# Kernel tuning notes

Hardware: AMD Instinct MI355X
Metric: run time of the kernel (lower is better)

The kernel has to match this reference:

```python
import jax, jax.numpy as jnp
import numpy as np
import math

HIDDEN = 1024
NUM_HEADS = 16
NUM_GROUPS = 16  # source einsum/rearrange only shape-checks when groups == heads
HEAD_DIM = HIDDEN // NUM_HEADS


def rope(x, base=10000.0):
    # x: [b, s, d]; applied to the FULL hidden vector before head split, as in source.
    # Source rope_fn has a reshape bug; this is the intended rotate-half RoPE with
    # half_d frequencies 1/base^(i/half_d) (== 1/base^(2i/d)).
    b, s, d = x.shape
    half = d // 2
    x1, x2 = x[..., :half], x[..., half:]
    pos = jnp.arange(s, dtype=x.dtype)[:, None]                          # [s,1]
    inv_freq = 1.0 / (base ** (jnp.arange(half, dtype=x.dtype) / half))  # [half]
    ang = pos * inv_freq[None, :]                                        # [s,half]
    sin = jnp.sin(ang)[None]                                             # [1,s,half]
    cos = jnp.cos(ang)[None]
    return jnp.concatenate([x1 * cos - x2 * sin, x2 * cos + x1 * sin], axis=-1)


def setup_inputs() -> dict:
    key = jax.random.key(0)
    ks = jax.random.split(key, 10)
    scale = 1.0 / math.sqrt(HIDDEN)
    inp = {
        "x": jax.random.normal(ks[0], (2, 2048, HIDDEN), dtype=jnp.float32),
        "attn_mask": jax.random.randint(ks[1], (2, 2048), 0, 2, dtype=jnp.int32),
        "Wq": jax.random.uniform(ks[2], (HIDDEN, HIDDEN), jnp.float32, -scale, scale),
        "bq": jax.random.uniform(ks[3], (HIDDEN,), jnp.float32, -scale, scale),
        "Wk": jax.random.uniform(ks[4], (HIDDEN, HIDDEN), jnp.float32, -scale, scale),
        "bk": jax.random.uniform(ks[5], (HIDDEN,), jnp.float32, -scale, scale),
        "Wv": jax.random.uniform(ks[6], (HIDDEN, HIDDEN), jnp.float32, -scale, scale),
        "bv": jax.random.uniform(ks[7], (HIDDEN,), jnp.float32, -scale, scale),
        "Wo": jax.random.uniform(ks[8], (HIDDEN, HIDDEN), jnp.float32, -scale, scale),
        "bo": jax.random.uniform(ks[9], (HIDDEN,), jnp.float32, -scale, scale),
    }
    return inp


def reference(x, attn_mask, Wq, bq, Wk, bk, Wv, bv, Wo, bo):
    b, s, _ = x.shape
    g = NUM_GROUPS
    subh = NUM_HEADS // g  # = 1 here
    d = HIDDEN // g        # per-group dim (== head dim when g == h)

    q = rope(x @ Wq.T + bq)
    k = rope(x @ Wk.T + bk)
    v = x @ Wv.T + bv

    # q: b s (g subh d) -> b g subh s d ; k,v: b s (g d) -> b g s d
    q = q.reshape(b, s, g, subh, d).transpose(0, 2, 3, 1, 4)
    k = k.reshape(b, s, g, d).transpose(0, 2, 1, 3)
    v = v.reshape(b, s, g, d).transpose(0, 2, 1, 3)

    e = jnp.einsum('bghqd,bgkd->bghqk', q, k) / math.sqrt(HEAD_DIM)  # [b,g,subh,s,s]
    mask5 = attn_mask[:, None, None, None, :]  # broadcast over g, subh, query
    e = jnp.where(mask5 == 0, -jnp.inf, e)
    attn = jax.nn.softmax(e, axis=-1)
    out = jnp.einsum('bghqk,bgkd->bghqd', attn, v)            # [b,g,subh,s,d]
    out = out.transpose(0, 3, 1, 2, 4).reshape(b, s, HIDDEN)  # b s (g subh d)
    return out @ Wo.T + bo
```

## Files before the change

### kernel.cpp

```cpp
#include <hip/hip_runtime.h>
#include <hip/hip_bf16.h>


constexpr int Bb  = 2;
constexpr int Ss  = 2048;
constexpr int Hh  = 1024;
constexpr int NHh = 16;
constexpr int Mm  = Bb * Ss;

typedef __attribute__((ext_vector_type(8))) unsigned short ushort8;
typedef __attribute__((ext_vector_type(4))) unsigned short ushort4_t;
typedef __attribute__((ext_vector_type(8))) short short8;
typedef __attribute__((ext_vector_type(4))) float f32x4;

__device__ __forceinline__ unsigned short f2bf(float f) {
    unsigned int u = __float_as_uint(f);
    u += 0x7fffu + ((u >> 16) & 1u);
    return (unsigned short)(u >> 16);
}
__device__ __forceinline__ float bf2f(unsigned short h) {
    return __uint_as_float(((unsigned int)h) << 16);
}
__device__ __forceinline__ void gload16(const void* g, void* l) {
    __builtin_amdgcn_global_load_lds(
        (const __attribute__((address_space(1))) unsigned int*)g,
        (__attribute__((address_space(3))) unsigned int*)l, 16, 0, 0);
}

__global__ __launch_bounds__(256) void convert_k(
    const float* __restrict__ x,
    const float* __restrict__ Wq, const float* __restrict__ Wk,
    const float* __restrict__ Wv, const float* __restrict__ Wo,
    unsigned short* __restrict__ xb, unsigned short* __restrict__ wall)
{
    size_t e = ((size_t)blockIdx.x * 256 + threadIdx.x) << 3;
    const float* s; unsigned short* d;
    if (e < (size_t)Mm * Hh) {
        s = x + e; d = xb + e;
    } else {
        size_t f = e - (size_t)Mm * Hh;
        int t = (int)(f >> 20);
        const float* w = (t == 0) ? Wq : (t == 1) ? Wk : (t == 2) ? Wv : Wo;
        s = w + (f & 1048575);
        d = wall + f;
    }
    float4 a = *(const float4*)s;
    float4 b = *(const float4*)(s + 4);
    ushort8 o;
    o[0] = f2bf(a.x); o[1] = f2bf(a.y); o[2] = f2bf(a.z); o[3] = f2bf(a.w);
    o[4] = f2bf(b.x); o[5] = f2bf(b.y); o[6] = f2bf(b.z); o[7] = f2bf(b.w);
    *(ushort8*)d = o;
}

#define GEMM_BODY(ATYPE_PTR, WPTR, K0MAX)                                          \
    __shared__ unsigned short As[128 * 64];                                        \
    __shared__ unsigned short Bs[128 * 64];                                        \
    const int tid  = threadIdx.x;                                                  \
    const int lane = tid & 63;                                                     \
    const int w    = tid >> 6;                                                     \
    const int wr   = w >> 1, wc = w & 1;                                           \
    const int l16  = lane & 15, g = lane >> 4;                                     \
    const int R0   = blockIdx.x * 128;                                             \
    char* asb = (char*)As; char* bsb = (char*)Bs;                                  \
    f32x4 acc[4][4] = {};                                                          \
    for (int k0 = 0; k0 < K0MAX; k0 += 64) {                                       \
        _Pragma("unroll")                                                          \
        for (int it = 0; it < 4; ++it) {                                           \
            int sbase = w * 4096 + it * 1024;                                      \
            int boff  = sbase + lane * 16;                                         \
            int r     = boff >> 7;                                                 \
            int c     = (boff >> 4) & 7;                                           \
            int col   = k0 + ((c ^ (r & 7)) << 3);                                 \
            gload16(&ATYPE_PTR[(size_t)(R0 + r) * 1024 + col], asb + sbase);       \
            gload16(&WPTR[(size_t)(gn + r) * 1024 + col], bsb + sbase);            \
        }                                                                          \
        __syncthreads();                                                           \
        short8 bfrag[4][2];                                                        \
        _Pragma("unroll")                                                          \
        for (int u = 0; u < 4; ++u) {                                              \
            int row = wc * 64 + u * 16 + l16;                                      \
            _Pragma("unroll")                                                      \
            for (int s = 0; s < 2; ++s)                                            \
                bfrag[u][s] = *(const short8*)(bsb + row * 128 +                   \
                               ((s * 64 + g * 16) ^ ((row & 7) << 4)));            \
        }                                                                          \
        _Pragma("unroll")                                                          \
        for (int t = 0; t < 4; ++t) {                                              \
            int row = wr * 64 + t * 16 + l16;                                      \
            short8 af[2];                                                          \
            _Pragma("unroll")                                                      \
            for (int s = 0; s < 2; ++s)                                            \
                af[s] = *(const short8*)(asb + row * 128 +                         \
                         ((s * 64 + g * 16) ^ ((row & 7) << 4)));                  \
            _Pragma("unroll")                                                      \
            for (int u = 0; u < 4; ++u) {                                          \
                acc[t][u] = __builtin_amdgcn_mfma_f32_16x16x32_bf16(af[0], bfrag[u][0], acc[t][u], 0, 0, 0); \
                acc[t][u] = __builtin_amdgcn_mfma_f32_16x16x32_bf16(af[1], bfrag[u][1], acc[t][u], 0, 0, 0); \
            }                                                                      \
        }                                                                          \
        __syncthreads();                                                           \
    }

__global__ __launch_bounds__(256) void gemm_qkv_k(
    const unsigned short* __restrict__ xb, const unsigned short* __restrict__ wall,
    const float* __restrict__ bq, const float* __restrict__ bk, const float* __restrict__ bv,
    unsigned short* __restrict__ q, unsigned short* __restrict__ k2,
    unsigned short* __restrict__ v)
{
    const int gn = blockIdx.y * 128;
    GEMM_BODY(xb, wall, 1024)

    const int sel = gn >> 10;
    const int n0  = gn & 1023;
    const float* bias = (sel == 0) ? bq : (sel == 1) ? bk : bv;
    unsigned short* outp = (sel == 0) ? q : (sel == 1) ? k2 : v;
    const float qs = (sel == 0) ? 0.18033688011112042f : 1.0f;
    #pragma unroll
    for (int u = 0; u < 4; ++u) {
        int coll = wc * 64 + u * 16 + l16;
        float bb = bias[n0 + coll];
        #pragma unroll
        for (int t = 0; t < 4; ++t)
            #pragma unroll
            for (int rr = 0; rr < 4; ++rr) {
                int row = R0 + wr * 64 + t * 16 + g * 4 + rr;
                outp[(size_t)row * 1024 + n0 + coll] = f2bf((acc[t][u][rr] + bb) * qs);
            }
    }
}

__global__ __launch_bounds__(256) void gemm_out_k(
    const unsigned short* __restrict__ ao, const unsigned short* __restrict__ wo,
    const float* __restrict__ bo, float* __restrict__ out)
{
    const int gn = blockIdx.y * 128;
    GEMM_BODY(ao, wo, 1024)

    #pragma unroll
    for (int u = 0; u < 4; ++u) {
        int coll = wc * 64 + u * 16 + l16;
        float bb = bo[gn + coll];
        #pragma unroll
        for (int t = 0; t < 4; ++t)
            #pragma unroll
            for (int rr = 0; rr < 4; ++rr) {
                int row = R0 + wr * 64 + t * 16 + g * 4 + rr;
                out[(size_t)row * 1024 + gn + coll] = acc[t][u][rr] + bb;
            }
    }
}

__global__ __launch_bounds__(256) void rope_k(
    unsigned short* __restrict__ q, unsigned short* __restrict__ kk)
{
    int idx = blockIdx.x * 256 + threadIdx.x;
    int row = idx >> 7;
    int j4  = (idx & 127) << 2;
    int pos = row & (Ss - 1);
    size_t base = (size_t)row * 1024;

    ushort4_t qa = *(ushort4_t*)&q[base + j4];
    ushort4_t qb = *(ushort4_t*)&q[base + 512 + j4];
    ushort4_t ka = *(ushort4_t*)&kk[base + j4];
    ushort4_t kb = *(ushort4_t*)&kk[base + 512 + j4];

    #pragma unroll
    for (int t = 0; t < 4; ++t) {
        float jj = (float)(j4 + t);
        float inv = exp2f(jj * -0.0259525632621414f);
        float ang = (float)pos * inv;
        float sn, cs;
        __sincosf(ang, &sn, &cs);
        float a = bf2f(qa[t]), b = bf2f(qb[t]);
        qa[t] = f2bf(a * cs - b * sn);
        qb[t] = f2bf(b * cs + a * sn);
        float c = bf2f(ka[t]), d = bf2f(kb[t]);
        ka[t] = f2bf(c * cs - d * sn);
        kb[t] = f2bf(d * cs + c * sn);
    }
    *(ushort4_t*)&q[base + j4]        = qa;
    *(ushort4_t*)&q[base + 512 + j4]  = qb;
    *(ushort4_t*)&kk[base + j4]       = ka;
    *(ushort4_t*)&kk[base + 512 + j4] = kb;
}

__global__ __launch_bounds__(256, 4) void flash_k(
    const unsigned short* __restrict__ q, const unsigned short* __restrict__ k,
    const unsigned short* __restrict__ v, const int* __restrict__ mask,
    unsigned short* __restrict__ ao)
{
    __shared__ unsigned short Ks[64 * 64];
    __shared__ unsigned short Vt[64 * 64];
    __shared__ unsigned short Pb[4][16 * 64];

    const int F   = blockIdx.x;
    const int xcd = F & 7, j = F >> 3;
    const int grp = xcd * 4 + (j >> 5);
    const int qb  = j & 31;
    const int h   = grp & 15;
    const int bz  = grp >> 4;

    const int tid  = threadIdx.x;
    const int lane = tid & 63;
    const int w    = tid >> 6;
    const int l16  = lane & 15;
    const int g    = lane >> 4;
    const int sw   = (lane & 7) << 4;

    char* ksb = (char*)&Ks[0];
    char* vtb = (char*)&Vt[0];
    char* pbb = (char*)&Pb[w][0];

    const int qrowbase = bz * Ss + qb * 64 + w * 16;

    short8 qf[2];
    #pragma unroll
    for (int s = 0; s < 2; ++s)
        qf[s] = *(const short8*)&q[(size_t)(qrowbase + l16) * 1024
                                   + h * 64 + s * 32 + g * 8];

    f32x4 O[4];
    #pragma unroll
    for (int d = 0; d < 4; ++d) O[d] = (f32x4)0.f;
    f32x4 Osum = (f32x4)0.f;
    float mrow = -1.0e4f;

    const float THR = 10.0f;

    short8 ones;
    #pragma unroll
    for (int e = 0; e < 8; ++e) ones[e] = (short)0x3F80;

    for (int kt = 0; kt < Ss / 64; ++kt) {
        #pragma unroll
        for (int it = 0; it < 2; ++it) {
            int cid = w * 128 + it * 64 + lane;
            int row = cid >> 3;
            int sub = cid & 7;
            gload16(&k[(size_t)(bz * Ss + kt * 64 + row) * 1024 + h * 64
                       + ((sub ^ (row & 7)) << 3)],
                    ksb + w * 2048 + it * 1024);
        }
        {
            int kv    = tid & 63;
            int dbase = (tid >> 6) << 4;
            #pragma unroll
            for (int half = 0; half < 2; ++half) {
                int d0 = dbase + half * 8;
                ushort8 t8 = *(const ushort8*)&v[(size_t)(bz * Ss + kt * 64 + kv) * 1024
                                                 + h * 64 + d0];
                #pragma unroll
                for (int jj = 0; jj < 8; ++jj) {
                    int d = d0 + jj;
                    *(unsigned short*)(vtb + d * 128 + ((kv * 2) ^ ((d & 7) << 4))) = t8[jj];
                }
            }
        }
        __syncthreads();

        f32x4 S[4];
        #pragma unroll
        for (int kt4 = 0; kt4 < 4; ++kt4) S[kt4] = (f32x4)0.f;
        #pragma unroll
        for (int kt4 = 0; kt4 < 4; ++kt4) {
            int key = kt4 * 16 + l16;
            short8 kf0 = *(const short8*)(ksb + key * 128 + ((g * 16) ^ sw));
            short8 kf1 = *(const short8*)(ksb + key * 128 + ((64 + g * 16) ^ sw));
            S[kt4] = __builtin_amdgcn_mfma_f32_16x16x32_bf16(kf0, qf[0], S[kt4], 0, 0, 0);
            S[kt4] = __builtin_amdgcn_mfma_f32_16x16x32_bf16(kf1, qf[1], S[kt4], 0, 0, 0);
        }

        int mk[4][4];
        #pragma unroll
        for (int kt4 = 0; kt4 < 4; ++kt4)
            *(int4*)&mk[kt4][0] = *(const int4*)&mask[bz * Ss + kt * 64 + kt4 * 16 + g * 4];
        #pragma unroll
        for (int kt4 = 0; kt4 < 4; ++kt4)
            #pragma unroll
            for (int r = 0; r < 4; ++r)
                S[kt4][r] = mk[kt4][r] ? S[kt4][r] : -1e30f;

        float m0 = fmaxf(fmaxf(S[0][0], S[0][1]), fmaxf(S[0][2], S[0][3]));
        float m1 = fmaxf(fmaxf(S[1][0], S[1][1]), fmaxf(S[1][2], S[1][3]));
        float m2 = fmaxf(fmaxf(S[2][0], S[2][1]), fmaxf(S[2][2], S[2][3]));
        float m3 = fmaxf(fmaxf(S[3][0], S[3][1]), fmaxf(S[3][2], S[3][3]));
        float m  = fmaxf(fmaxf(m0, m1), fmaxf(m2, m3));
        m = fmaxf(m, __shfl_xor(m, 16));
        m = fmaxf(m, __shfl_xor(m, 32));

        if (__any((int)(m > mrow + THR))) {
            float mn = fmaxf(mrow, m);
            float rs = exp2f(mrow - mn);
            mrow = mn;
            #pragma unroll
            for (int r = 0; r < 4; ++r) {
                float f0 = __shfl(rs, g * 4 + r);
                #pragma unroll
                for (int dt = 0; dt < 4; ++dt) O[dt][r] *= f0;
                Osum[r] *= f0;
            }
        }

        #pragma unroll
        for (int kt4 = 0; kt4 < 4; ++kt4) {
            float p0 = exp2f(S[kt4][0] - mrow);
            float p1 = exp2f(S[kt4][1] - mrow);
            float p2 = exp2f(S[kt4][2] - mrow);
            float p3 = exp2f(S[kt4][3] - mrow);
            unsigned int u01, u23;
            asm("v_cvt_pk_bf16_f32 %0, %1, %2" : "=v"(u01) : "v"(p0), "v"(p1));
            asm("v_cvt_pk_bf16_f32 %0, %1, %2" : "=v"(u23) : "v"(p2), "v"(p3));
            int pbyte = (kt4 * 32 + g * 8) ^ ((l16 & 7) << 4);
            *(uint2*)(pbb + l16 * 128 + pbyte) = make_uint2(u01, u23);
        }

        #pragma unroll
        for (int ks = 0; ks < 2; ++ks) {
            short8 pf = *(const short8*)(pbb + l16 * 128 + ((ks * 64 + g * 16) ^ sw));
            Osum = __builtin_amdgcn_mfma_f32_16x16x32_bf16(pf, ones, Osum, 0, 0, 0);
            #pragma unroll
            for (int dt = 0; dt < 4; ++dt) {
                short8 vf = *(const short8*)(vtb + (dt * 16 + l16) * 128 + ((ks * 64 + g * 16) ^ sw));
                O[dt] = __builtin_amdgcn_mfma_f32_16x16x32_bf16(pf, vf, O[dt], 0, 0, 0);
            }
        }
        __syncthreads();
    }

    #pragma unroll
    for (int r = 0; r < 4; ++r) {
        float inv = 1.0f / Osum[r];
        int row = qrowbase + g * 4 + r;
        #pragma unroll
        for (int dt = 0; dt < 4; ++dt)
            ao[(size_t)row * 1024 + h * 64 + dt * 16 + l16] = f2bf(O[dt][r] * inv);
    }
}

extern "C" void kernel_launch(void* const* d_in, const int* in_sizes, int n_in,
                              void* d_out, int out_size, void* d_ws, size_t ws_size,
                              hipStream_t stream)
{
    const float* x  = (const float*)d_in[0];
    const int*   am = (const int*)d_in[1];
    const float* Wq = (const float*)d_in[2];
    const float* bq = (const float*)d_in[3];
    const float* Wk = (const float*)d_in[4];
    const float* bk = (const float*)d_in[5];
    const float* Wv = (const float*)d_in[6];
    const float* bv = (const float*)d_in[7];
    const float* Wo = (const float*)d_in[8];
    const float* bo = (const float*)d_in[9];
    float* out = (float*)d_out;

    const size_t NE = (size_t)Mm * Hh;
    unsigned short* q    = (unsigned short*)d_ws;
    unsigned short* k    = q + NE;
    unsigned short* v    = k + NE;
    unsigned short* ao   = v + NE;
    unsigned short* xb   = ao + NE;
    unsigned short* wall = xb + NE;
    unsigned short* wo   = wall + 3u * 1048576u;

    convert_k<<<(2 * NE) / (256 * 8), 256, 0, stream>>>(x, Wq, Wk, Wv, Wo, xb, wall);
    gemm_qkv_k<<<dim3(Mm / 128, 3072 / 128), 256, 0, stream>>>(
        xb, wall, bq, bk, bv, q, k, v);
    rope_k<<<(Mm * 128) / 256, 256, 0, stream>>>(q, k);
    flash_k<<<dim3(Ss / 64 * NHh * Bb), 256, 0, stream>>>(q, k, v, am, ao);
    gemm_out_k<<<dim3(Mm / 128, Hh / 128), 256, 0, stream>>>(ao, wo, bo, out);
}
```

Measured before the change: 168.2 us.

## Pre-swizzle Q/K/V into MFMA fragment layout and register-pipeline flash attention

RoPE now also writes Q and K into an MFMA-fragment-ordered buffer, and a new kernel reorders V into transposed fragment order. This lets flash attention load K/V fragments straight from global memory into registers, double-buffering K across iterations, with no LDS and no barriers. Each warp now handles two 16-row query tiles (128 rows per block). P is repacked in registers with permlane swaps instead of an LDS round trip. The costs are an extra V pass, more workspace aliasing, higher register pressure (launch bounds min blocks lowered to 2), and half as many flash blocks.

Result: no change. 166.5 us (-1.0%).

```diff
diff --git a/kernel.cpp b/kernel.cpp
--- a/kernel.cpp
+++ b/kernel.cpp
@@ -9,9 +9,9 @@
 constexpr int Mm  = Bb * Ss;
 
 typedef __attribute__((ext_vector_type(8))) unsigned short ushort8;
-typedef __attribute__((ext_vector_type(4))) unsigned short ushort4_t;
 typedef __attribute__((ext_vector_type(8))) short short8;
 typedef __attribute__((ext_vector_type(4))) float f32x4;
+typedef __attribute__((ext_vector_type(4))) unsigned int u32x4;
 
 __device__ __forceinline__ unsigned short f2bf(float f) {
     unsigned int u = __float_as_uint(f);
@@ -150,53 +150,192 @@
     }
 }
 
-__global__ __launch_bounds__(256) void rope_k(
-    unsigned short* __restrict__ q, unsigned short* __restrict__ kk)
-{
-    int idx = blockIdx.x * 256 + threadIdx.x;
-    int row = idx >> 7;
-    int j4  = (idx & 127) << 2;
-    int pos = row & (Ss - 1);
-    size_t base = (size_t)row * 1024;
-
-    ushort4_t qa = *(ushort4_t*)&q[base + j4];
-    ushort4_t qb = *(ushort4_t*)&q[base + 512 + j4];
-    ushort4_t ka = *(ushort4_t*)&kk[base + j4];
-    ushort4_t kb = *(ushort4_t*)&kk[base + 512 + j4];
-
-    #pragma unroll
-    for (int t = 0; t < 4; ++t) {
-        float jj = (float)(j4 + t);
+__global__ __launch_bounds__(256) void rope_frag_k(
+    const unsigned short* __restrict__ qin, const unsigned short* __restrict__ kin,
+    unsigned short* __restrict__ qfrag, unsigned short* __restrict__ kfrag)
+{
+    __shared__ unsigned short Ld[2][64][72];
+    const int kt = blockIdx.x;
+    const int hp = blockIdx.y;
+    const int zz = blockIdx.z;
+    const int bz = zz & 1, sel = zz >> 1;
+    const unsigned short* src = sel ? kin : qin;
+    unsigned short* dstf = sel ? kfrag : qfrag;
+
+    const int t   = threadIdx.x;
+    const int r   = t & 63;
+    const int c16 = (t >> 6) << 4;
+    const int pos = kt * 64 + r;
+    const size_t rowb = (size_t)(bz * Ss + pos) * 1024;
+
+    ushort8 A0 = *(const ushort8*)&src[rowb + hp * 64 + c16];
+    ushort8 A1 = *(const ushort8*)&src[rowb + hp * 64 + c16 + 8];
+    ushort8 B0 = *(const ushort8*)&src[rowb + (hp + 8) * 64 + c16];
+    ushort8 B1 = *(const ushort8*)&src[rowb + (hp + 8) * 64 + c16 + 8];
+
+    #pragma unroll
+    for (int i = 0; i < 16; ++i) {
+        int d = c16 + i;
+        float jj  = (float)(hp * 64 + d);
         float inv = exp2f(jj * -0.0259525632621414f);
         float ang = (float)pos * inv;
         float sn, cs;
         __sincosf(ang, &sn, &cs);
-        float a = bf2f(qa[t]), b = bf2f(qb[t]);
-        qa[t] = f2bf(a * cs - b * sn);
-        qb[t] = f2bf(b * cs + a * sn);
-        float c = bf2f(ka[t]), d = bf2f(kb[t]);
-        ka[t] = f2bf(c * cs - d * sn);
-        kb[t] = f2bf(d * cs + c * sn);
-    }
-    *(ushort4_t*)&q[base + j4]        = qa;
-    *(ushort4_t*)&q[base + 512 + j4]  = qb;
-    *(ushort4_t*)&kk[base + j4]       = ka;
-    *(ushort4_t*)&kk[base + 512 + j4] = kb;
-}
-
-__global__ __launch_bounds__(256, 4) void flash_k(
-    const unsigned short* __restrict__ q, const unsigned short* __restrict__ k,
-    const unsigned short* __restrict__ v, const int* __restrict__ mask,
+        unsigned short ua = (i < 8) ? A0[i] : A1[i - 8];
+        unsigned short ub = (i < 8) ? B0[i] : B1[i - 8];
+        float a = bf2f(ua), b = bf2f(ub);
+        Ld[0][r][d] = f2bf(a * cs - b * sn);
+        Ld[1][r][d] = f2bf(b * cs + a * sn);
+    }
+    __syncthreads();
+
+    #pragma unroll
+    for (int cc = 0; cc < 4; ++cc) {
+        int c    = t * 4 + cc;
+        int hh   = c >> 9;
+        int ci   = c & 511;
+        int blk  = ci >> 7, s2 = (ci >> 6) & 1, lane2 = ci & 63;
+        int gg = lane2 >> 4, ll = lane2 & 15;
+        ushort8 o = *(const ushort8*)&Ld[hh][blk * 16 + ll][s2 * 32 + gg * 8];
+        size_t base = (size_t)(bz * 16 + hp + hh * 8) * 131072 + (size_t)kt * 4096;
+        *(ushort8*)&dstf[base + (size_t)ci * 8] = o;
+    }
+}
+
+__global__ __launch_bounds__(256) void fragify_v_k(
+    const unsigned short* __restrict__ v, unsigned short* __restrict__ vfrag)
+{
+    __shared__ unsigned short Ld[64][72];
+    const int kt = blockIdx.x, bh = blockIdx.y;
+    const int bz = bh >> 4, h = bh & 15;
+    const int t = threadIdx.x;
+    const int r = t & 63, c0 = (t >> 6) << 4;
+    const unsigned short* srcp = &v[(size_t)(bz * Ss + kt * 64 + r) * 1024 + h * 64 + c0];
+    *(ushort8*)&Ld[r][c0]     = *(const ushort8*)srcp;
+    *(ushort8*)&Ld[r][c0 + 8] = *(const ushort8*)(srcp + 8);
+    __syncthreads();
+
+    #pragma unroll
+    for (int cc = 0; cc < 2; ++cc) {
+        int c = t * 2 + cc;
+        int dt4 = c >> 7, ks = (c >> 6) & 1, lane2 = c & 63;
+        int gg = lane2 >> 4, ll = lane2 & 15;
+        ushort8 o;
+        #pragma unroll
+        for (int e = 0; e < 8; ++e)
+            o[e] = Ld[ks * 32 + gg * 8 + e][dt4 * 16 + ll];
+        *(ushort8*)&vfrag[(size_t)bh * 131072 + (size_t)kt * 4096 + (size_t)c * 8] = o;
+    }
+}
+
+#define FLASH_ITER(KC, KN, KT)                                                     \
+    {                                                                              \
+        const int ktn = ((KT) + 1) & 31;                                           \
+        _Pragma("unroll")                                                          \
+        for (int i = 0; i < 8; ++i)                                                \
+            KN[i] = *(const short8*)&kfb[(size_t)ktn * 4096 + i * 512 + lane * 8]; \
+        _Pragma("unroll")                                                          \
+        for (int i = 0; i < 8; ++i)                                                \
+            VV[i] = *(const short8*)&vfb[(size_t)(KT) * 4096 + i * 512 + lane * 8];\
+        int mk[4][4];                                                              \
+        _Pragma("unroll")                                                          \
+        for (int k4 = 0; k4 < 4; ++k4)                                             \
+            *(int4*)&mk[k4][0] =                                                   \
+                *(const int4*)&mask[bz * Ss + (KT) * 64 + k4 * 16 + g * 4];        \
+        f32x4 S[2][4];                                                             \
+        _Pragma("unroll")                                                          \
+        for (int t = 0; t < 2; ++t)                                                \
+            _Pragma("unroll")                                                      \
+            for (int k4 = 0; k4 < 4; ++k4) S[t][k4] = (f32x4)0.f;                  \
+        _Pragma("unroll")                                                          \
+        for (int k4 = 0; k4 < 4; ++k4)                                             \
+            _Pragma("unroll")                                                      \
+            for (int t = 0; t < 2; ++t) {                                          \
+                S[t][k4] = __builtin_amdgcn_mfma_f32_16x16x32_bf16(                \
+                    KC[k4 * 2 + 0], qf[t][0], S[t][k4], 0, 0, 0);                  \
+                S[t][k4] = __builtin_amdgcn_mfma_f32_16x16x32_bf16(                \
+                    KC[k4 * 2 + 1], qf[t][1], S[t][k4], 0, 0, 0);                  \
+            }                                                                      \
+        _Pragma("unroll")                                                          \
+        for (int t = 0; t < 2; ++t)                                                \
+            _Pragma("unroll")                                                      \
+            for (int k4 = 0; k4 < 4; ++k4)                                         \
+                _Pragma("unroll")                                                  \
+                for (int r = 0; r < 4; ++r)                                        \
+                    S[t][k4][r] = mk[k4][r] ? S[t][k4][r] : -1e30f;                \
+        float rm[2];                                                               \
+        _Pragma("unroll")                                                          \
+        for (int t = 0; t < 2; ++t) {                                              \
+            float m0 = fmaxf(fmaxf(S[t][0][0], S[t][0][1]), fmaxf(S[t][0][2], S[t][0][3])); \
+            float m1 = fmaxf(fmaxf(S[t][1][0], S[t][1][1]), fmaxf(S[t][1][2], S[t][1][3])); \
+            float m2 = fmaxf(fmaxf(S[t][2][0], S[t][2][1]), fmaxf(S[t][2][2], S[t][2][3])); \
+            float m3 = fmaxf(fmaxf(S[t][3][0], S[t][3][1]), fmaxf(S[t][3][2], S[t][3][3])); \
+            float m  = fmaxf(fmaxf(m0, m1), fmaxf(m2, m3));                        \
+            m = fmaxf(m, __shfl_xor(m, 16));                                       \
+            m = fmaxf(m, __shfl_xor(m, 32));                                       \
+            rm[t] = m;                                                             \
+        }                                                                          \
+        bool grow = (rm[0] > mrow[0] + 10.0f) || (rm[1] > mrow[1] + 10.0f);        \
+        if (__any((int)grow)) {                                                    \
+            float mn0 = fmaxf(mrow[0], rm[0]);                                     \
+            float mn1 = fmaxf(mrow[1], rm[1]);                                     \
+            float rs0 = exp2f(mrow[0] - mn0);                                      \
+            float rs1 = exp2f(mrow[1] - mn1);                                      \
+            mrow[0] = mn0; mrow[1] = mn1;                                          \
+            _Pragma("unroll")                                                      \
+            for (int r = 0; r < 4; ++r) {                                          \
+                float f0 = __shfl(rs0, g * 4 + r);                                 \
+                float f1 = __shfl(rs1, g * 4 + r);                                 \
+                _Pragma("unroll")                                                  \
+                for (int dt = 0; dt < 4; ++dt) { O[0][dt][r] *= f0; O[1][dt][r] *= f1; } \
+                Osum[0][r] *= f0; Osum[1][r] *= f1;                                \
+            }                                                                      \
+        }                                                                          \
+        _Pragma("unroll")                                                          \
+        for (int t = 0; t < 2; ++t) {                                              \
+            unsigned int U[4][2];                                                  \
+            _Pragma("unroll")                                                      \
+            for (int k4 = 0; k4 < 4; ++k4) {                                       \
+                float p0 = exp2f(S[t][k4][0] - mrow[t]);                           \
+                float p1 = exp2f(S[t][k4][1] - mrow[t]);                           \
+                float p2 = exp2f(S[t][k4][2] - mrow[t]);                           \
+                float p3 = exp2f(S[t][k4][3] - mrow[t]);                           \
+                asm("v_cvt_pk_bf16_f32 %0, %1, %2" : "=v"(U[k4][0]) : "v"(p0), "v"(p1)); \
+                asm("v_cvt_pk_bf16_f32 %0, %1, %2" : "=v"(U[k4][1]) : "v"(p2), "v"(p3)); \
+            }                                                                      \
+                \
+            asm("v_permlane32_swap_b32 %0, %1" : "+v"(U[0][0]), "+v"(U[1][0]));    \
+            asm("v_permlane32_swap_b32 %0, %1" : "+v"(U[0][1]), "+v"(U[1][1]));    \
+            asm("v_permlane32_swap_b32 %0, %1" : "+v"(U[2][0]), "+v"(U[3][0]));    \
+            asm("v_permlane32_swap_b32 %0, %1" : "+v"(U[2][1]), "+v"(U[3][1]));    \
+            asm("v_permlane16_swap_b32 %0, %1" : "+v"(U[0][0]), "+v"(U[1][0]));    \
+            asm("v_permlane16_swap_b32 %0, %1" : "+v"(U[0][1]), "+v"(U[1][1]));    \
+            asm("v_permlane16_swap_b32 %0, %1" : "+v"(U[2][0]), "+v"(U[3][0]));    \
+            asm("v_permlane16_swap_b32 %0, %1" : "+v"(U[2][1]), "+v"(U[3][1]));    \
+            _Pragma("unroll")                                                      \
+            for (int ks = 0; ks < 2; ++ks) {                                       \
+                u32x4 gp;                                                          \
+                gp[0] = U[2 * ks][0]; gp[1] = U[2 * ks][1];                        \
+                gp[2] = U[2 * ks + 1][0]; gp[3] = U[2 * ks + 1][1];                \
+                short8 pf = __builtin_bit_cast(short8, gp);                        \
+                Osum[t] = __builtin_amdgcn_mfma_f32_16x16x32_bf16(pf, ones, Osum[t], 0, 0, 0); \
+                _Pragma("unroll")                                                  \
+                for (int dt = 0; dt < 4; ++dt)                                     \
+                    O[t][dt] = __builtin_amdgcn_mfma_f32_16x16x32_bf16(            \
+                        pf, VV[dt * 2 + ks], O[t][dt], 0, 0, 0);                   \
+            }                                                                      \
+        }                                                                          \
+    }
+
+__global__ __launch_bounds__(256, 2) void flash_k(
+    const unsigned short* __restrict__ qfrag, const unsigned short* __restrict__ kfrag,
+    const unsigned short* __restrict__ vfrag, const int* __restrict__ mask,
     unsigned short* __restrict__ ao)
 {
-    __shared__ unsigned short Ks[64 * 64];
-    __shared__ unsigned short Vt[64 * 64];
-    __shared__ unsigned short Pb[4][16 * 64];
-
     const int F   = blockIdx.x;
     const int xcd = F & 7, j = F >> 3;
-    const int grp = xcd * 4 + (j >> 5);
-    const int qb  = j & 31;
+    const int grp = xcd * 4 + (j >> 4);
+    const int qb  = j & 15;
     const int h   = grp & 15;
     const int bz  = grp >> 4;
 
@@ -205,136 +344,55 @@
     const int w    = tid >> 6;
     const int l16  = lane & 15;
     const int g    = lane >> 4;
-    const int sw   = (lane & 7) << 4;
-
-    char* ksb = (char*)&Ks[0];
-    char* vtb = (char*)&Vt[0];
-    char* pbb = (char*)&Pb[w][0];
-
-    const int qrowbase = bz * Ss + qb * 64 + w * 16;
-
-    short8 qf[2];
-    #pragma unroll
-    for (int s = 0; s < 2; ++s)
-        qf[s] = *(const short8*)&q[(size_t)(qrowbase + l16) * 1024
-                                   + h * 64 + s * 32 + g * 8];
-
-    f32x4 O[4];
-    #pragma unroll
-    for (int d = 0; d < 4; ++d) O[d] = (f32x4)0.f;
-    f32x4 Osum = (f32x4)0.f;
-    float mrow = -1.0e4f;
-
-    const float THR = 10.0f;
+
+    const size_t fb = (size_t)(bz * 16 + h) * 131072;
+    const unsigned short* kfb = kfrag + fb;
+    const unsigned short* vfb = vfrag + fb;
+    const unsigned short* qfb = qfrag + fb;
+
+    const int qrowbase = bz * Ss + qb * 128 + w * 32;
+
+    short8 qf[2][2];
+    #pragma unroll
+    for (int t = 0; t < 2; ++t)
+        #pragma unroll
+        for (int s = 0; s < 2; ++s)
+            qf[t][s] = *(const short8*)&qfb[(size_t)(qb * 8 + w * 2 + t) * 1024
+                                            + s * 512 + lane * 8];
+
+    f32x4 O[2][4];
+    #pragma unroll
+    for (int t = 0; t < 2; ++t)
+        #pragma unroll
+        for (int d = 0; d < 4; ++d) O[t][d] = (f32x4)0.f;
+    f32x4 Osum[2];
+    Osum[0] = (f32x4)0.f; Osum[1] = (f32x4)0.f;
+    float mrow[2] = {-1.0e4f, -1.0e4f};
 
     short8 ones;
     #pragma unroll
     for (int e = 0; e < 8; ++e) ones[e] = (short)0x3F80;
 
-    for (int kt = 0; kt < Ss / 64; ++kt) {
-        #pragma unroll
-        for (int it = 0; it < 2; ++it) {
-            int cid = w * 128 + it * 64 + lane;
-            int row = cid >> 3;
-            int sub = cid & 7;
-            gload16(&k[(size_t)(bz * Ss + kt * 64 + row) * 1024 + h * 64
-                       + ((sub ^ (row & 7)) << 3)],
-                    ksb + w * 2048 + it * 1024);
+    short8 KA[8], KB[8], VV[8];
+    #pragma unroll
+    for (int i = 0; i < 8; ++i)
+        KA[i] = *(const short8*)&kfb[(size_t)i * 512 + lane * 8];
+
+    for (int kt = 0; kt < 32; kt += 2) {
+        FLASH_ITER(KA, KB, kt)
+        FLASH_ITER(KB, KA, kt + 1)
+    }
+
+    #pragma unroll
+    for (int t = 0; t < 2; ++t)
+        #pragma unroll
+        for (int r = 0; r < 4; ++r) {
+            float inv = 1.0f / Osum[t][r];
+            int row = qrowbase + t * 16 + g * 4 + r;
+            #pragma unroll
+            for (int dt = 0; dt < 4; ++dt)
+                ao[(size_t)row * 1024 + h * 64 + dt * 16 + l16] = f2bf(O[t][dt][r] * inv);
         }
-        {
-            int kv    = tid & 63;
-            int dbase = (tid >> 6) << 4;
-            #pragma unroll
-            for (int half = 0; half < 2; ++half) {
-                int d0 = dbase + half * 8;
-                ushort8 t8 = *(const ushort8*)&v[(size_t)(bz * Ss + kt * 64 + kv) * 1024
-                                                 + h * 64 + d0];
-                #pragma unroll
-                for (int jj = 0; jj < 8; ++jj) {
-                    int d = d0 + jj;
-                    *(unsigned short*)(vtb + d * 128 + ((kv * 2) ^ ((d & 7) << 4))) = t8[jj];
-                }
-            }
-        }
-        __syncthreads();
-
-        f32x4 S[4];
-        #pragma unroll
-        for (int kt4 = 0; kt4 < 4; ++kt4) S[kt4] = (f32x4)0.f;
-        #pragma unroll
-        for (int kt4 = 0; kt4 < 4; ++kt4) {
-            int key = kt4 * 16 + l16;
-            short8 kf0 = *(const short8*)(ksb + key * 128 + ((g * 16) ^ sw));
-            short8 kf1 = *(const short8*)(ksb + key * 128 + ((64 + g * 16) ^ sw));
-            S[kt4] = __builtin_amdgcn_mfma_f32_16x16x32_bf16(kf0, qf[0], S[kt4], 0, 0, 0);
-            S[kt4] = __builtin_amdgcn_mfma_f32_16x16x32_bf16(kf1, qf[1], S[kt4], 0, 0, 0);
-        }
-
-        int mk[4][4];
-        #pragma unroll
-        for (int kt4 = 0; kt4 < 4; ++kt4)
-            *(int4*)&mk[kt4][0] = *(const int4*)&mask[bz * Ss + kt * 64 + kt4 * 16 + g * 4];
-        #pragma unroll
-        for (int kt4 = 0; kt4 < 4; ++kt4)
-            #pragma unroll
-            for (int r = 0; r < 4; ++r)
-                S[kt4][r] = mk[kt4][r] ? S[kt4][r] : -1e30f;
-
-        float m0 = fmaxf(fmaxf(S[0][0], S[0][1]), fmaxf(S[0][2], S[0][3]));
-        float m1 = fmaxf(fmaxf(S[1][0], S[1][1]), fmaxf(S[1][2], S[1][3]));
-        float m2 = fmaxf(fmaxf(S[2][0], S[2][1]), fmaxf(S[2][2], S[2][3]));
-        float m3 = fmaxf(fmaxf(S[3][0], S[3][1]), fmaxf(S[3][2], S[3][3]));
-        float m  = fmaxf(fmaxf(m0, m1), fmaxf(m2, m3));
-        m = fmaxf(m, __shfl_xor(m, 16));
-        m = fmaxf(m, __shfl_xor(m, 32));
-
-        if (__any((int)(m > mrow + THR))) {
-            float mn = fmaxf(mrow, m);
-            float rs = exp2f(mrow - mn);
-            mrow = mn;
-            #pragma unroll
-            for (int r = 0; r < 4; ++r) {
-                float f0 = __shfl(rs, g * 4 + r);
-                #pragma unroll
-                for (int dt = 0; dt < 4; ++dt) O[dt][r] *= f0;
-                Osum[r] *= f0;
-            }
-        }
-
-        #pragma unroll
-        for (int kt4 = 0; kt4 < 4; ++kt4) {
-            float p0 = exp2f(S[kt4][0] - mrow);
-            float p1 = exp2f(S[kt4][1] - mrow);
-            float p2 = exp2f(S[kt4][2] - mrow);
-            float p3 = exp2f(S[kt4][3] - mrow);
-            unsigned int u01, u23;
-            asm("v_cvt_pk_bf16_f32 %0, %1, %2" : "=v"(u01) : "v"(p0), "v"(p1));
-            asm("v_cvt_pk_bf16_f32 %0, %1, %2" : "=v"(u23) : "v"(p2), "v"(p3));
-            int pbyte = (kt4 * 32 + g * 8) ^ ((l16 & 7) << 4);
-            *(uint2*)(pbb + l16 * 128 + pbyte) = make_uint2(u01, u23);
-        }
-
-        #pragma unroll
-        for (int ks = 0; ks < 2; ++ks) {
-            short8 pf = *(const short8*)(pbb + l16 * 128 + ((ks * 64 + g * 16) ^ sw));
-            Osum = __builtin_amdgcn_mfma_f32_16x16x32_bf16(pf, ones, Osum, 0, 0, 0);
-            #pragma unroll
-            for (int dt = 0; dt < 4; ++dt) {
-                short8 vf = *(const short8*)(vtb + (dt * 16 + l16) * 128 + ((ks * 64 + g * 16) ^ sw));
-                O[dt] = __builtin_amdgcn_mfma_f32_16x16x32_bf16(pf, vf, O[dt], 0, 0, 0);
-            }
-        }
-        __syncthreads();
-    }
-
-    #pragma unroll
-    for (int r = 0; r < 4; ++r) {
-        float inv = 1.0f / Osum[r];
-        int row = qrowbase + g * 4 + r;
-        #pragma unroll
-        for (int dt = 0; dt < 4; ++dt)
-            ao[(size_t)row * 1024 + h * 64 + dt * 16 + l16] = f2bf(O[dt][r] * inv);
-    }
 }
 
 extern "C" void kernel_launch(void* const* d_in, const int* in_sizes, int n_in,
@@ -354,18 +412,22 @@
     float* out = (float*)d_out;
 
     const size_t NE = (size_t)Mm * Hh;
-    unsigned short* q    = (unsigned short*)d_ws;
-    unsigned short* k    = q + NE;
-    unsigned short* v    = k + NE;
-    unsigned short* ao   = v + NE;
-    unsigned short* xb   = ao + NE;
-    unsigned short* wall = xb + NE;
-    unsigned short* wo   = wall + 3u * 1048576u;
+    unsigned short* q     = (unsigned short*)d_ws;
+    unsigned short* k     = q + NE;
+    unsigned short* v     = k + NE;
+    unsigned short* ao    = v + NE;
+    unsigned short* xb    = ao + NE;
+    unsigned short* wall  = xb + NE;
+    unsigned short* wo    = wall + 3u * 1048576u;
+    unsigned short* kfrag = wall + 4u * 1048576u;
+    unsigned short* qfrag = xb;
+    unsigned short* vfrag = q;
 
     convert_k<<<(2 * NE) / (256 * 8), 256, 0, stream>>>(x, Wq, Wk, Wv, Wo, xb, wall);
     gemm_qkv_k<<<dim3(Mm / 128, 3072 / 128), 256, 0, stream>>>(
         xb, wall, bq, bk, bv, q, k, v);
-    rope_k<<<(Mm * 128) / 256, 256, 0, stream>>>(q, k);
-    flash_k<<<dim3(Ss / 64 * NHh * Bb), 256, 0, stream>>>(q, k, v, am, ao);
+    rope_frag_k<<<dim3(32, 8, 4), 256, 0, stream>>>(q, k, qfrag, kfrag);
+    fragify_v_k<<<dim3(32, 32), 256, 0, stream>>>(v, vfrag);
+    flash_k<<<dim3(512), 256, 0, stream>>>(qfrag, kfrag, vfrag, am, ao);
     gemm_out_k<<<dim3(Mm / 128, Hh / 128), 256, 0, stream>>>(ao, wo, bo, out);
 }
```
